# Kernel tuning notes

Measured on AMD Instinct MI355X. Metric: run time of the kernel, lower is better.

## Reference

```python
import jax, jax.numpy as jnp
import numpy as np

B, L, D = 2, 2048, 1024
H = 16
C = 128            # chunk_size
N = L // C         # num chunks
SCALE = float(np.sqrt(D))  # softmax_scale = sqrt(d_model)


def setup_inputs() -> dict:
    key = jax.random.key(0)
    ks = jax.random.split(key, 5)
    return {
        "x": jax.random.normal(ks[0], (B, L, D), dtype=jnp.float32),
        "w_qkv": jax.random.normal(ks[1], (D, 3 * D), dtype=jnp.float32) * (1.0 / np.sqrt(D)),
        "b_qkv": jax.random.normal(ks[2], (3 * D,), dtype=jnp.float32) * 0.02,
        "w_o": jax.random.normal(ks[3], (D, D), dtype=jnp.float32) * (1.0 / np.sqrt(D)),
        "b_o": jax.random.normal(ks[4], (D,), dtype=jnp.float32) * 0.02,
    }


def reference(x, w_qkv, b_qkv, w_o, b_o):
    b, l, d = x.shape
    hd = d // H
    qkv = x @ w_qkv + b_qkv                         # (B,L,3D)
    q, k, v = jnp.split(qkv, 3, axis=-1)
    q = q.reshape(b, l, H, hd)
    k = k.reshape(b, l, H, hd)
    v = v.reshape(b, l, H, hd)

    q_chunks = q.reshape(b, N, C, H, hd)
    k_chunks = k.reshape(b, N, C, H, hd)
    # mean_pool over the chunk dim
    q_pool = q_chunks.mean(axis=2)                  # (B,N,H,hd)
    k_pool = k_chunks.mean(axis=2)

    token2chunk = jnp.einsum('blhd,bnhd->bhln', q, k_pool)          # (B,H,L,N)
    chunk2token = jnp.einsum('bnhd,bnchd->bhnc', q_pool, k_chunks)  # (B,H,N,C)
    # outer product over (n,c) -> full (B,H,L,L) score matrix
    A = token2chunk[..., :, None] * chunk2token[:, :, None, :, :]   # (B,H,L,N,C)
    A = A.reshape(b, H, l, l)

    # direct intra-chunk attention overwrites the diagonal blocks
    direct = jnp.einsum('bnqhd,bnkhd->bhnqk', q_chunks, k_chunks)   # (B,H,N,C,C)
    A6 = A.reshape(b, H, N, C, N, C)
    eye = jnp.eye(N, dtype=bool)[:, None, :, None]                  # (N,1,N,1)
    A6 = jnp.where(eye, direct[:, :, :, :, None, :], A6)
    A = A6.reshape(b, H, l, l)

    # causal mask applied multiplicatively (masked scores become 0, NOT -inf)
    causal = jnp.tril(jnp.ones((l, l), dtype=bool))
    A = jnp.where(causal, A, 0.0) / SCALE
    A = jax.nn.softmax(A, axis=-1)

    out = jnp.einsum('bhqv,bvhd->bhqd', A, v)       # (B,H,L,hd)
    out = out.transpose(0, 2, 1, 3).reshape(b, l, d)
    return out @ w_o + b_o
```

## Files before the change

kernel.cpp:

```cpp
#include <hip/hip_runtime.h>
#include <math.h>

#define B_   2
#define L_   2048
#define D_   1024
#define H_   16
#define HD_  64
#define C_   128
#define N_   16
#define INV_SCALE 0.03125f

typedef _Float16 h8 __attribute__((ext_vector_type(8)));
typedef _Float16 h4 __attribute__((ext_vector_type(4)));
typedef float    f4 __attribute__((ext_vector_type(4)));

#define MFMA16(a, b, c) __builtin_amdgcn_mfma_f32_16x16x32_f16((a), (b), (c), 0, 0, 0)

__device__ __forceinline__ void gl_lds16(const void* g, void* l) {
  __builtin_amdgcn_global_load_lds(
      (const __attribute__((address_space(1))) void*)g,
      (__attribute__((address_space(3))) void*)l, 16, 0, 0);
}

__global__ __launch_bounds__(256) void cvtx_kernel(const float* __restrict__ X,
                                                   _Float16* __restrict__ Xh)
{
  int i = (blockIdx.x * 256 + threadIdx.x) * 4;
  float4 v = *(const float4*)(X + i);
  h4 o = { (_Float16)v.x, (_Float16)v.y, (_Float16)v.z, (_Float16)v.w };
  *(h4*)(Xh + i) = o;
}

__global__ __launch_bounds__(256) void wt_kernel(const float* __restrict__ W,
                                                 _Float16* __restrict__ WT,
                                                 int Nc, int Kd)
{
  __shared__ float ts[32][36];
  const int tid = threadIdx.x;
  const int n0 = blockIdx.x * 32, k0 = blockIdx.y * 32;
  {
    int kr = tid >> 3, nc4 = (tid & 7) * 4;
    float4 v = *(const float4*)&W[(size_t)(k0 + kr) * Nc + n0 + nc4];
    ts[kr][nc4+0] = v.x; ts[kr][nc4+1] = v.y; ts[kr][nc4+2] = v.z; ts[kr][nc4+3] = v.w;
  }
  __syncthreads();
  {
    int nr = tid >> 3, kc4 = (tid & 7) * 4;
    h4 o = { (_Float16)ts[kc4+0][nr], (_Float16)ts[kc4+1][nr],
             (_Float16)ts[kc4+2][nr], (_Float16)ts[kc4+3][nr] };
    *(h4*)&WT[(size_t)(n0 + nr) * Kd + k0 + kc4] = o;
  }
}

template<int MT>
__global__ __launch_bounds__(256, 4) void gemm16_kernel(
    const _Float16* __restrict__ A, const _Float16* __restrict__ Bt,
    const float* __restrict__ bias,
    _Float16* __restrict__ Qh, _Float16* __restrict__ Kh, _Float16* __restrict__ VT,
    float* __restrict__ out,
    float* __restrict__ QP, float* __restrict__ KP, float* __restrict__ VCS,
    int Kd, int mode)
{
  constexpr int SM = MT / 32;
  __shared__ __align__(16) _Float16 As[2][MT * 32];
  __shared__ __align__(16) _Float16 Bs[2][4096];
  __shared__ float cred[2][128];
  const int tid = threadIdx.x;
  const int lane = tid & 63, w = tid >> 6;
  const int q = lane >> 4, r = lane & 15;
  const int mb = (w >> 1) * (MT / 2);
  const int nb = (w & 1) * 64;

  int m0, n0;
  {
    const int id = blockIdx.x;
    const int xcd = id & 7, slot = id >> 3;
    if constexpr (MT == 128) {
      n0 = (xcd * 3 + (slot % 3)) * 128;
      m0 = (slot / 3) * 128;
    } else {
      n0 = xcd * 128;
      m0 = slot * 64;
    }
  }

  const int Rr = tid >> 2;
  const int cd = (tid & 3) ^ ((Rr >> 1) & 3);
  const _Float16* Ag = A + (size_t)(m0 + Rr) * Kd + cd * 8;
  const _Float16* Bg = Bt + (size_t)(n0 + Rr) * Kd + cd * 8;
  const size_t rowStep = (size_t)64 * Kd;

  f4 acc[SM][4];
  #pragma unroll
  for (int s = 0; s < SM; ++s)
    #pragma unroll
    for (int t = 0; t < 4; ++t) acc[s][t] = (f4){0.f, 0.f, 0.f, 0.f};

  const int nIter = Kd >> 5;
  const int koff = (q ^ ((r >> 1) & 3)) << 3;

  auto stage = [&](int bf, int kt) {
    _Float16* Asl = &As[bf][w * 512];
    _Float16* Bsl = &Bs[bf][w * 512];
    gl_lds16(Ag + kt, Asl);
    if constexpr (MT == 128) gl_lds16(Ag + kt + rowStep, Asl + 2048);
    gl_lds16(Bg + kt, Bsl);
    gl_lds16(Bg + kt + rowStep, Bsl + 2048);
  };

  stage(0, 0);

  for (int it = 0; it < nIter; ++it) {
    __syncthreads();
    if (it + 1 < nIter) stage((it + 1) & 1, (it + 1) << 5);
    const _Float16* Ab = As[it & 1];
    const _Float16* Bb = Bs[it & 1];
    h8 af[SM], bf4[4];
    #pragma unroll
    for (int s = 0; s < SM; ++s)
      af[s] = *(const h8*)&Ab[(mb + s * 16 + r) * 32 + koff];
    #pragma unroll
    for (int t = 0; t < 4; ++t)
      bf4[t] = *(const h8*)&Bb[(nb + t * 16 + r) * 32 + koff];
    #pragma unroll
    for (int s = 0; s < SM; ++s)
      #pragma unroll
      for (int t = 0; t < 4; ++t)
        acc[s][t] = MFMA16(af[s], bf4[t], acc[s][t]);
  }

  if (mode == 0) {
    #pragma unroll
    for (int t = 0; t < 4; ++t) {
      int gn = n0 + nb + t * 16 + r;
      float bj = bias[gn];
      int which = gn >> 10, rem = gn & 1023;
      int h2 = rem >> 6, d2 = rem & 63;
      if (which < 2) {
        _Float16* dst = which == 0 ? Qh : Kh;
        #pragma unroll
        for (int s = 0; s < SM; ++s)
          #pragma unroll
          for (int i = 0; i < 4; ++i) {
            int gm = m0 + mb + s * 16 + q * 4 + i;
            int b2 = gm >> 11, l2 = gm & 2047;
            dst[(((size_t)(b2 * H_ + h2)) * L_ + l2) * HD_ + d2] =
                (_Float16)(acc[s][t][i] + bj);
          }
      } else {
        #pragma unroll
        for (int s = 0; s < SM; ++s) {
          int gm0 = m0 + mb + s * 16 + q * 4;
          int b2 = gm0 >> 11, l2 = gm0 & 2047;
          h4 hv = { (_Float16)(acc[s][t][0] + bj), (_Float16)(acc[s][t][1] + bj),
                    (_Float16)(acc[s][t][2] + bj), (_Float16)(acc[s][t][3] + bj) };
          *(h4*)&VT[((size_t)(b2 * H_ + h2) * HD_ + d2) * L_ + l2] = hv;
        }
      }
    }
    float colsum[4];
    #pragma unroll
    for (int t = 0; t < 4; ++t) {
      float s2 = 0.f;
      #pragma unroll
      for (int s = 0; s < SM; ++s)
        #pragma unroll
        for (int i = 0; i < 4; ++i) s2 += acc[s][t][i];
      s2 += __shfl_xor(s2, 16);
      s2 += __shfl_xor(s2, 32);
      colsum[t] = s2;
    }
    if (q == 0) {
      #pragma unroll
      for (int t = 0; t < 4; ++t)
        cred[w >> 1][nb + t * 16 + r] = colsum[t];
    }
    __syncthreads();
    if (tid < 128) {
      int j = tid;
      float ssum = cred[0][j] + cred[1][j];
      int gn = n0 + j;
      float bj = bias[gn];
      int which = gn >> 10, rem = gn & 1023;
      int h2 = rem >> 6, d2 = rem & 63;
      int b2 = m0 >> 11, nch = (m0 & 2047) >> 7;
      size_t o = (((size_t)(b2 * H_ + h2)) * N_ + nch) * HD_ + d2;
      if (which == 0)      QP[o] = ssum * (1.f / 128.f) + bj;
      else if (which == 1) KP[o] = ssum * (1.f / 128.f) + bj;
      else                 VCS[o] = ssum + 128.f * bj;
    }
  } else {
    #pragma unroll
    for (int t = 0; t < 4; ++t) {
      int gn = n0 + nb + t * 16 + r;
      float bj = bias[gn];
      #pragma unroll
      for (int s = 0; s < SM; ++s)
        #pragma unroll
        for (int i = 0; i < 4; ++i) {
          int gm = m0 + mb + s * 16 + q * 4 + i;
          out[(size_t)gm * 1024 + gn] = acc[s][t][i] + bj;
        }
    }
  }
}

__global__ void csuf_kernel(const float* __restrict__ VCS, float* __restrict__ CSUF)
{
  int bh = blockIdx.x, d = threadIdx.x;
  float run = 0.f;
  for (int n = N_ - 1; n >= 0; --n) {
    size_t o = ((size_t)bh * N_ + n) * HD_ + d;
    CSUF[o] = run;
    run += VCS[o];
  }
}

__global__ __launch_bounds__(128) void c2t_kernel(
    const float* __restrict__ QP, const _Float16* __restrict__ Kh,
    float* __restrict__ C2T, float* __restrict__ C2TMX, float* __restrict__ C2TMN)
{
  __shared__ float qp_s[64];
  __shared__ float red[4];
  int bh = blockIdx.x >> 4, n = blockIdx.x & 15, tid = threadIdx.x;
  int w = tid >> 6, lane = tid & 63;
  if (tid < 64) qp_s[tid] = QP[((size_t)bh * N_ + n) * HD_ + tid];
  const _Float16* kr = Kh + (((size_t)bh * L_) + n * C_ + tid) * HD_;
  h8 kv[8];
  #pragma unroll
  for (int c8 = 0; c8 < 8; ++c8) kv[c8] = *(const h8*)(kr + c8 * 8);
  __syncthreads();
  float s = 0.f;
  #pragma unroll
  for (int c8 = 0; c8 < 8; ++c8)
    #pragma unroll
    for (int j = 0; j < 8; ++j)
      s = fmaf((float)kv[c8][j], qp_s[c8 * 8 + j], s);
  C2T[((size_t)bh * N_ + n) * C_ + tid] = s;
  float mx = s, mn = s;
  #pragma unroll
  for (int st = 1; st <= 32; st <<= 1) {
    mx = fmaxf(mx, __shfl_xor(mx, st));
    mn = fminf(mn, __shfl_xor(mn, st));
  }
  if (lane == 0) { red[w * 2] = mx; red[w * 2 + 1] = mn; }
  __syncthreads();
  if (tid == 0) {
    C2TMX[bh * N_ + n] = fmaxf(red[0], red[2]);
    C2TMN[bh * N_ + n] = fminf(red[1], red[3]);
  }
}

__global__ __launch_bounds__(256, 4) void attn3_kernel(
    const _Float16* __restrict__ Qh, const _Float16* __restrict__ Kh,
    const _Float16* __restrict__ VT,
    const float* __restrict__ C2T, const float* __restrict__ C2TMX,
    const float* __restrict__ C2TMN, const float* __restrict__ CSUF,
    const float* __restrict__ KP, _Float16* __restrict__ AOh)
{
  __shared__ __align__(16) _Float16 kv_s[2][8192];
  __shared__ __align__(16) _Float16 kp_s[1024];
  __shared__ __align__(16) float c2t_s[2][128];

  const int tid = threadIdx.x;
  const int w = tid >> 6, lane = tid & 63;
  const int q = lane >> 4, r = lane & 15;
  const int r7 = r & 7;
  const int id = blockIdx.x;
  const int bh = ((id & 7) << 2) + ((id >> 3) & 3);
  const int qt = 31 - (id >> 5);
  const int l0 = qt * 64;
  const int nq = l0 >> 7;
  const int off = l0 & 127;
  const int rowA = l0 + w * 16 + r;
  const int pcw = off + w * 16 + r;
  const size_t bhL = (size_t)bh * L_;
  const int b2 = bh >> 4, h2 = bh & 15;

  auto stageV = [&](int bf, int n) {
    #pragma unroll
    for (int j = 0; j < 4; ++j) {
      int f = j * 256 + tid;
      int d = f >> 4, p = f & 15;
      int c16 = p ^ (d & 7);
      gl_lds16(VT + ((size_t)bh * HD_ + d) * L_ + n * C_ + c16 * 8,
               &kv_s[bf][(size_t)(j * 256 + w * 64) * 8]);
    }
  };
  auto stageK = [&](int bf, int n) {
    #pragma unroll
    for (int j = 0; j < 4; ++j) {
      int f = j * 256 + tid;
      int c = f >> 3, p = f & 7;
      int ck = p ^ (c & 7);
      gl_lds16(Kh + (bhL + n * C_ + c) * HD_ + ck * 8,
               &kv_s[bf][(size_t)(j * 256 + w * 64) * 8]);
    }
  };
  auto stageC = [&](int bf, int n) {
    if (tid < 32)
      gl_lds16(C2T + ((size_t)bh * N_ + n) * C_ + lane * 4, &c2t_s[bf][0]);
  };

  {
    int n4 = tid >> 4, d4 = (tid & 15) * 4;
    float4 kpv = *(const float4*)&KP[((size_t)bh * N_ + n4) * HD_ + d4];
    int sd = ((((d4 >> 3) ^ (n4 & 7)) << 3) | (d4 & 7));
    h4 hv = { (_Float16)kpv.x, (_Float16)kpv.y, (_Float16)kpv.z, (_Float16)kpv.w };
    *(h4*)&kp_s[n4 * 64 + sd] = hv;
  }
  h8 qa0 = *(const h8*)(Qh + (bhL + rowA) * HD_ + q * 8);
  h8 qa1 = *(const h8*)(Qh + (bhL + rowA) * HD_ + 32 + q * 8);
  float mxL = C2TMX[bh * N_ + (lane & 15)];
  float mnL = C2TMN[bh * N_ + (lane & 15)];
  stageK(0, nq);
  __syncthreads();

  f4 tvacc = (f4){0.f, 0.f, 0.f, 0.f};
  {
    h8 kpa0 = *(const h8*)&kp_s[r * 64 + ((q ^ r7) << 3)];
    h8 kpa1 = *(const h8*)&kp_s[r * 64 + (((4 + q) ^ r7) << 3)];
    tvacc = MFMA16(kpa0, qa0, tvacc);
    tvacc = MFMA16(kpa1, qa1, tvacc);
  }
  float tvs[4];
  #pragma unroll
  for (int i = 0; i < 4; ++i) tvs[i] = tvacc[i] * INV_SCALE;

  float pm = -1e30f;
  #pragma unroll
  for (int i = 0; i < 4; ++i) {
    int n = q * 4 + i;
    float mx = __shfl(mxL, n);
    float mn = __shfl(mnL, n);
    float cm = fmaxf(tvs[i] * mx, tvs[i] * mn);
    pm = (n < nq) ? fmaxf(pm, cm) : pm;
  }
  pm = fmaxf(pm, __shfl_xor(pm, 16));
  pm = fmaxf(pm, __shfl_xor(pm, 32));

  f4 sc[8];
  #pragma unroll
  for (int u = 0; u < 8; ++u) sc[u] = (f4){0.f, 0.f, 0.f, 0.f};
  #pragma unroll
  for (int u = 0; u < 8; ++u) {
    h8 kb0 = *(const h8*)&kv_s[0][(u * 16 + r) * 64 + ((q ^ r7) << 3)];
    h8 kb1 = *(const h8*)&kv_s[0][(u * 16 + r) * 64 + (((4 + q) ^ r7) << 3)];
    sc[u] = MFMA16(qa0, kb0, sc[u]);
    sc[u] = MFMA16(qa1, kb1, sc[u]);
  }
  stageV(1, nq);

  float rm[4] = {-1e30f, -1e30f, -1e30f, -1e30f};
  #pragma unroll
  for (int u = 0; u < 8; ++u) {
    int col = nq * C_ + u * 16 + r;
    #pragma unroll
    for (int i = 0; i < 4; ++i) {
      int row = l0 + w * 16 + q * 4 + i;
      float v = sc[u][i] * INV_SCALE;
      v = (col <= row) ? v : -1e30f;
      sc[u][i] = v;
      rm[i] = fmaxf(rm[i], v);
    }
  }
  #pragma unroll
  for (int i = 0; i < 4; ++i) {
    rm[i] = fmaxf(rm[i], __shfl_xor(rm[i], 1));
    rm[i] = fmaxf(rm[i], __shfl_xor(rm[i], 2));
    rm[i] = fmaxf(rm[i], __shfl_xor(rm[i], 4));
    rm[i] = fmaxf(rm[i], __shfl_xor(rm[i], 8));
  }
  const int srcl = (r >> 2) << 4;
  const int ri = r & 3;
  float t0 = __shfl(rm[0], srcl), t1 = __shfl(rm[1], srcl);
  float t2 = __shfl(rm[2], srcl), t3 = __shfl(rm[3], srcl);
  float myrm = ri == 0 ? t0 : ri == 1 ? t1 : ri == 2 ? t2 : t3;

  const float M = fmaxf(fmaxf(pm, myrm), 0.f);
  const float e0 = __expf(-M);
  float Mc[4];
  #pragma unroll
  for (int i = 0; i < 4; ++i) Mc[i] = __shfl(M, (q << 2) + i);

  float cs[4] = {0.f, 0.f, 0.f, 0.f};
  #pragma unroll
  for (int u = 0; u < 8; ++u)
    #pragma unroll
    for (int i = 0; i < 4; ++i) {
      float v = sc[u][i];
      float p = (v > -1e29f) ? __expf(v - Mc[i]) : 0.f;
      sc[u][i] = p;
      cs[i] += p;
    }
  #pragma unroll
  for (int i = 0; i < 4; ++i) {
    cs[i] += __shfl_xor(cs[i], 1);
    cs[i] += __shfl_xor(cs[i], 2);
    cs[i] += __shfl_xor(cs[i], 4);
    cs[i] += __shfl_xor(cs[i], 8);
  }
  float c0 = __shfl(cs[0], srcl), c1 = __shfl(cs[1], srcl);
  float c2 = __shfl(cs[2], srcl), c3 = __shfl(cs[3], srcl);
  float den = ri == 0 ? c0 : ri == 1 ? c1 : ri == 2 ? c2 : c3;

  __syncthreads();
  _Float16* pw = &kv_s[0][w * 2048];
  #pragma unroll
  for (int u = 0; u < 8; ++u)
    #pragma unroll
    for (int i = 0; i < 4; ++i) {
      int row = q * 4 + i, col = u * 16 + r;
      pw[row * 128 + ((((col >> 3) ^ (row & 7)) << 3) | (col & 7))] =
          (_Float16)sc[u][i];
    }

  f4 oacc[4], sacc[4];
  #pragma unroll
  for (int t = 0; t < 4; ++t) {
    oacc[t] = (f4){0.f, 0.f, 0.f, 0.f};
    sacc[t] = (f4){0.f, 0.f, 0.f, 0.f};
  }
  #pragma unroll
  for (int s = 0; s < 4; ++s) {
    h8 pa = *(const h8*)&pw[r * 128 + (((s * 4 + q) ^ r7) << 3)];
    h8 mk;
    #pragma unroll
    for (int j2 = 0; j2 < 8; ++j2)
      mk[j2] = (_Float16)((s * 32 + q * 8 + j2 > pcw) ? 1.f : 0.f);
    #pragma unroll
    for (int t = 0; t < 4; ++t) {
      h8 vb = *(const h8*)&kv_s[1][(t * 16 + r) * 128 + (((s * 4 + q) ^ r7) << 3)];
      oacc[t] = MFMA16(pa, vb, oacc[t]);
      sacc[t] = MFMA16(mk, vb, sacc[t]);
    }
  }

  __syncthreads();
  if (nq >= 1) { stageV(0, nq - 1); stageC(0, nq - 1); }

  for (int n = nq - 1; n >= 0; --n) {
    const int cur = (nq - 1 - n) & 1, nxt = cur ^ 1;
    __syncthreads();
    if (n >= 1) { stageV(nxt, n - 1); stageC(nxt, n - 1); }
    int i0 = n & 3;
    float tvx = i0 == 0 ? tvs[0] : i0 == 1 ? tvs[1] : i0 == 2 ? tvs[2] : tvs[3];
    float tvn = __shfl(tvx, ((n >> 2) << 4) + r);
    float csum = 0.f;
    #pragma unroll
    for (int s = 0; s < 4; ++s) {
      const float* cp = &c2t_s[cur][s * 32 + q * 8];
      float4 ca = *(const float4*)cp;
      float4 cb = *(const float4*)(cp + 4);
      float p0 = __expf(tvn * ca.x - M), p1 = __expf(tvn * ca.y - M);
      float p2 = __expf(tvn * ca.z - M), p3 = __expf(tvn * ca.w - M);
      float p4 = __expf(tvn * cb.x - M), p5 = __expf(tvn * cb.y - M);
      float p6 = __expf(tvn * cb.z - M), p7 = __expf(tvn * cb.w - M);
      csum += p0 + p1 + p2 + p3 + p4 + p5 + p6 + p7;
      h8 pa = { (_Float16)p0, (_Float16)p1, (_Float16)p2, (_Float16)p3,
                (_Float16)p4, (_Float16)p5, (_Float16)p6, (_Float16)p7 };
      #pragma unroll
      for (int t = 0; t < 4; ++t) {
        h8 vb = *(const h8*)&kv_s[cur][(t * 16 + r) * 128 + (((s * 4 + q) ^ r7) << 3)];
        oacc[t] = MFMA16(pa, vb, oacc[t]);
      }
    }
    csum += __shfl_xor(csum, 16);
    csum += __shfl_xor(csum, 32);
    den += csum;
  }

  int cnt = (L_ - 1) - rowA;
  den += e0 * (float)cnt;
  float e0r[4], dnr[4];
  #pragma unroll
  for (int i = 0; i < 4; ++i) {
    e0r[i] = __shfl(e0,  (q << 2) + i);
    dnr[i] = __shfl(den, (q << 2) + i);
  }
  #pragma unroll
  for (int t = 0; t < 4; ++t) {
    int d = t * 16 + r;
    float csf = CSUF[((size_t)bh * N_ + nq) * HD_ + d];
    #pragma unroll
    for (int i = 0; i < 4; ++i) {
      int row = l0 + w * 16 + q * 4 + i;
      float suffix = sacc[t][i] + csf;
      float o = (oacc[t][i] + e0r[i] * suffix) / dnr[i];
      AOh[((size_t)b2 * L_ + row) * D_ + h2 * HD_ + d] = (_Float16)o;
    }
  }
}

extern "C" void kernel_launch(void* const* d_in, const int* in_sizes, int n_in,
                              void* d_out, int out_size, void* d_ws, size_t ws_size,
                              hipStream_t stream)
{
  (void)in_sizes; (void)n_in; (void)out_size; (void)ws_size;
  const float* x     = (const float*)d_in[0];
  const float* w_qkv = (const float*)d_in[1];
  const float* b_qkv = (const float*)d_in[2];
  const float* w_o   = (const float*)d_in[3];
  const float* b_o   = (const float*)d_in[4];
  float* out = (float*)d_out;

  char* p = (char*)d_ws;
  _Float16* xh   = (_Float16*)p; p += (size_t)4194304 * 2;
  _Float16* wqT  = (_Float16*)p; p += (size_t)3145728 * 2;
  _Float16* woT  = (_Float16*)p; p += (size_t)1048576 * 2;
  _Float16* Qh   = (_Float16*)p; p += (size_t)4194304 * 2;
  _Float16* Kh   = (_Float16*)p; p += (size_t)4194304 * 2;
  _Float16* VT   = (_Float16*)p; p += (size_t)4194304 * 2;
  _Float16* AOh  = (_Float16*)p; p += (size_t)4194304 * 2;
  float*    C2T  = (float*)p;    p += (size_t)65536 * 4;
  float*    QP   = (float*)p;    p += (size_t)32768 * 4;
  float*    KP   = (float*)p;    p += (size_t)32768 * 4;
  float*    VCS  = (float*)p;    p += (size_t)32768 * 4;
  float*    CSUF = (float*)p;    p += (size_t)32768 * 4;
  float*    MXa  = (float*)p;    p += (size_t)512 * 4;
  float*    MNa  = (float*)p;    p += (size_t)512 * 4;

  cvtx_kernel<<<4096, 256, 0, stream>>>(x, xh);
  wt_kernel<<<dim3(96, 32), 256, 0, stream>>>(w_qkv, wqT, 3 * D_, D_);
  wt_kernel<<<dim3(32, 32), 256, 0, stream>>>(w_o, woT, D_, D_);
  gemm16_kernel<128><<<768, 256, 0, stream>>>(
      xh, wqT, b_qkv, Qh, Kh, VT, nullptr, QP, KP, VCS, D_, 0);
  csuf_kernel<<<B_ * H_, 64, 0, stream>>>(VCS, CSUF);
  c2t_kernel<<<B_ * H_ * N_, 128, 0, stream>>>(QP, Kh, C2T, MXa, MNa);
  attn3_kernel<<<1024, 256, 0, stream>>>(
      Qh, Kh, VT, C2T, MXa, MNa, CSUF, KP, AOh);
  gemm16_kernel<64><<<512, 256, 0, stream>>>(
      AOh, woT, b_o, nullptr, nullptr, nullptr, out, nullptr, nullptr, nullptr, D_, 1);
}
```

Before: 180.8 us.

## Merge prep and pooling launches, widen attention blocks to full 128-row chunks

```diff
diff --git a/kernel.cpp b/kernel.cpp
--- a/kernel.cpp
+++ b/kernel.cpp
@@ -22,22 +22,30 @@
       (__attribute__((address_space(3))) void*)l, 16, 0, 0);
 }
 
-__global__ __launch_bounds__(256) void cvtx_kernel(const float* __restrict__ X,
-                                                   _Float16* __restrict__ Xh)
-{
-  int i = (blockIdx.x * 256 + threadIdx.x) * 4;
-  float4 v = *(const float4*)(X + i);
-  h4 o = { (_Float16)v.x, (_Float16)v.y, (_Float16)v.z, (_Float16)v.w };
-  *(h4*)(Xh + i) = o;
-}
-
-__global__ __launch_bounds__(256) void wt_kernel(const float* __restrict__ W,
-                                                 _Float16* __restrict__ WT,
-                                                 int Nc, int Kd)
+__global__ __launch_bounds__(256) void prep_kernel(
+    const float* __restrict__ X, _Float16* __restrict__ Xh,
+    const float* __restrict__ Wq, _Float16* __restrict__ WqT,
+    const float* __restrict__ Wo, _Float16* __restrict__ WoT)
 {
   __shared__ float ts[32][36];
   const int tid = threadIdx.x;
-  const int n0 = blockIdx.x * 32, k0 = blockIdx.y * 32;
+  const int id = blockIdx.x;
+  if (id < 4096) {
+    int i = id * 1024 + tid * 4;
+    float4 v = *(const float4*)(X + i);
+    h4 o = { (_Float16)v.x, (_Float16)v.y, (_Float16)v.z, (_Float16)v.w };
+    *(h4*)(Xh + i) = o;
+    return;
+  }
+  const float* W; _Float16* WT; int Nc, bx, by;
+  if (id < 7168) {
+    int idx = id - 4096;
+    W = Wq; WT = WqT; Nc = 3072; bx = idx % 96; by = idx / 96;
+  } else {
+    int idx = id - 7168;
+    W = Wo; WT = WoT; Nc = 1024; bx = idx & 31; by = idx >> 5;
+  }
+  const int n0 = bx * 32, k0 = by * 32;
   {
     int kr = tid >> 3, nc4 = (tid & 7) * 4;
     float4 v = *(const float4*)&W[(size_t)(k0 + kr) * Nc + n0 + nc4];
@@ -48,7 +56,7 @@
     int nr = tid >> 3, kc4 = (tid & 7) * 4;
     h4 o = { (_Float16)ts[kc4+0][nr], (_Float16)ts[kc4+1][nr],
              (_Float16)ts[kc4+2][nr], (_Float16)ts[kc4+3][nr] };
-    *(h4*)&WT[(size_t)(n0 + nr) * Kd + k0 + kc4] = o;
+    *(h4*)&WT[(size_t)(n0 + nr) * 1024 + k0 + kc4] = o;
   }
 }
 
@@ -177,9 +185,9 @@
     }
     __syncthreads();
     if (tid < 128) {
-      int j = tid;
-      float ssum = cred[0][j] + cred[1][j];
-      int gn = n0 + j;
+      int jj = tid;
+      float ssum = cred[0][jj] + cred[1][jj];
+      int gn = n0 + jj;
       float bj = bias[gn];
       int which = gn >> 10, rem = gn & 1023;
       int h2 = rem >> 6, d2 = rem & 63;
@@ -205,23 +213,26 @@
   }
 }
 
-__global__ void csuf_kernel(const float* __restrict__ VCS, float* __restrict__ CSUF)
-{
-  int bh = blockIdx.x, d = threadIdx.x;
-  float run = 0.f;
-  for (int n = N_ - 1; n >= 0; --n) {
-    size_t o = ((size_t)bh * N_ + n) * HD_ + d;
-    CSUF[o] = run;
-    run += VCS[o];
-  }
-}
-
-__global__ __launch_bounds__(128) void c2t_kernel(
+__global__ __launch_bounds__(128) void pool2_kernel(
     const float* __restrict__ QP, const _Float16* __restrict__ Kh,
-    float* __restrict__ C2T, float* __restrict__ C2TMX, float* __restrict__ C2TMN)
+    const float* __restrict__ VCS,
+    float* __restrict__ C2T, float* __restrict__ C2TMX, float* __restrict__ C2TMN,
+    float* __restrict__ CSUF)
 {
   __shared__ float qp_s[64];
   __shared__ float red[4];
+  if (blockIdx.x >= 512) {
+    int bh = blockIdx.x - 512, d = threadIdx.x;
+    if (d < 64) {
+      float run = 0.f;
+      for (int n = N_ - 1; n >= 0; --n) {
+        size_t o = ((size_t)bh * N_ + n) * HD_ + d;
+        CSUF[o] = run;
+        run += VCS[o];
+      }
+    }
+    return;
+  }
   int bh = blockIdx.x >> 4, n = blockIdx.x & 15, tid = threadIdx.x;
   int w = tid >> 6, lane = tid & 63;
   if (tid < 64) qp_s[tid] = QP[((size_t)bh * N_ + n) * HD_ + tid];
@@ -251,14 +262,16 @@
   }
 }
 
-__global__ __launch_bounds__(256, 4) void attn3_kernel(
+__global__ __launch_bounds__(512, 4) void attn4_kernel(
     const _Float16* __restrict__ Qh, const _Float16* __restrict__ Kh,
     const _Float16* __restrict__ VT,
     const float* __restrict__ C2T, const float* __restrict__ C2TMX,
     const float* __restrict__ C2TMN, const float* __restrict__ CSUF,
     const float* __restrict__ KP, _Float16* __restrict__ AOh)
 {
-  __shared__ __align__(16) _Float16 kv_s[2][8192];
+  __shared__ __align__(16) _Float16 buf0[8192];
+  __shared__ __align__(16) _Float16 buf1[8192];
+  __shared__ __align__(16) _Float16 buf2[8192];
   __shared__ __align__(16) _Float16 kp_s[1024];
   __shared__ __align__(16) float c2t_s[2][128];
 
@@ -268,41 +281,39 @@
   const int r7 = r & 7;
   const int id = blockIdx.x;
   const int bh = ((id & 7) << 2) + ((id >> 3) & 3);
-  const int qt = 31 - (id >> 5);
-  const int l0 = qt * 64;
-  const int nq = l0 >> 7;
-  const int off = l0 & 127;
+  const int nq = 15 - (id >> 5);
+  const int l0 = nq * 128;
   const int rowA = l0 + w * 16 + r;
-  const int pcw = off + w * 16 + r;
+  const int pcw = w * 16 + r;
   const size_t bhL = (size_t)bh * L_;
   const int b2 = bh >> 4, h2 = bh & 15;
 
-  auto stageV = [&](int bf, int n) {
-    #pragma unroll
-    for (int j = 0; j < 4; ++j) {
-      int f = j * 256 + tid;
+  auto stageV = [&](_Float16* buf, int n) {
+    #pragma unroll
+    for (int j2 = 0; j2 < 2; ++j2) {
+      int f = j2 * 512 + tid;
       int d = f >> 4, p = f & 15;
       int c16 = p ^ (d & 7);
       gl_lds16(VT + ((size_t)bh * HD_ + d) * L_ + n * C_ + c16 * 8,
-               &kv_s[bf][(size_t)(j * 256 + w * 64) * 8]);
+               buf + (size_t)(j2 * 512 + w * 64) * 8);
     }
   };
-  auto stageK = [&](int bf, int n) {
-    #pragma unroll
-    for (int j = 0; j < 4; ++j) {
-      int f = j * 256 + tid;
+  auto stageK = [&](_Float16* buf, int n) {
+    #pragma unroll
+    for (int j2 = 0; j2 < 2; ++j2) {
+      int f = j2 * 512 + tid;
       int c = f >> 3, p = f & 7;
       int ck = p ^ (c & 7);
       gl_lds16(Kh + (bhL + n * C_ + c) * HD_ + ck * 8,
-               &kv_s[bf][(size_t)(j * 256 + w * 64) * 8]);
+               buf + (size_t)(j2 * 512 + w * 64) * 8);
     }
   };
   auto stageC = [&](int bf, int n) {
     if (tid < 32)
-      gl_lds16(C2T + ((size_t)bh * N_ + n) * C_ + lane * 4, &c2t_s[bf][0]);
+      gl_lds16(C2T + ((size_t)bh * N_ + n) * C_ + tid * 4, &c2t_s[bf][0]);
   };
 
-  {
+  if (tid < 256) {
     int n4 = tid >> 4, d4 = (tid & 15) * 4;
     float4 kpv = *(const float4*)&KP[((size_t)bh * N_ + n4) * HD_ + d4];
     int sd = ((((d4 >> 3) ^ (n4 & 7)) << 3) | (d4 & 7));
@@ -311,9 +322,11 @@
   }
   h8 qa0 = *(const h8*)(Qh + (bhL + rowA) * HD_ + q * 8);
   h8 qa1 = *(const h8*)(Qh + (bhL + rowA) * HD_ + 32 + q * 8);
-  float mxL = C2TMX[bh * N_ + (lane & 15)];
-  float mnL = C2TMN[bh * N_ + (lane & 15)];
-  stageK(0, nq);
+  float mxL = C2TMX[bh * N_ + r];
+  float mnL = C2TMN[bh * N_ + r];
+  stageK(buf0, nq);
+  stageV(buf2, nq);
+  if (nq >= 1) stageC(0, nq - 1);
   __syncthreads();
 
   f4 tvacc = (f4){0.f, 0.f, 0.f, 0.f};
@@ -344,22 +357,21 @@
   for (int u = 0; u < 8; ++u) sc[u] = (f4){0.f, 0.f, 0.f, 0.f};
   #pragma unroll
   for (int u = 0; u < 8; ++u) {
-    h8 kb0 = *(const h8*)&kv_s[0][(u * 16 + r) * 64 + ((q ^ r7) << 3)];
-    h8 kb1 = *(const h8*)&kv_s[0][(u * 16 + r) * 64 + (((4 + q) ^ r7) << 3)];
+    h8 kb0 = *(const h8*)&buf0[(u * 16 + r) * 64 + ((q ^ r7) << 3)];
+    h8 kb1 = *(const h8*)&buf0[(u * 16 + r) * 64 + (((4 + q) ^ r7) << 3)];
     sc[u] = MFMA16(qa0, kb0, sc[u]);
     sc[u] = MFMA16(qa1, kb1, sc[u]);
   }
-  stageV(1, nq);
 
   float rm[4] = {-1e30f, -1e30f, -1e30f, -1e30f};
   #pragma unroll
   for (int u = 0; u < 8; ++u) {
-    int col = nq * C_ + u * 16 + r;
+    int lcol = u * 16 + r;
     #pragma unroll
     for (int i = 0; i < 4; ++i) {
-      int row = l0 + w * 16 + q * 4 + i;
+      int lrow = w * 16 + q * 4 + i;
       float v = sc[u][i] * INV_SCALE;
-      v = (col <= row) ? v : -1e30f;
+      v = (lcol <= lrow) ? v : -1e30f;
       sc[u][i] = v;
       rm[i] = fmaxf(rm[i], v);
     }
@@ -405,7 +417,8 @@
   float den = ri == 0 ? c0 : ri == 1 ? c1 : ri == 2 ? c2 : c3;
 
   __syncthreads();
-  _Float16* pw = &kv_s[0][w * 2048];
+
+  _Float16* pw = (w < 4) ? (buf0 + w * 2048) : (buf1 + (w - 4) * 2048);
   #pragma unroll
   for (int u = 0; u < 8; ++u)
     #pragma unroll
@@ -430,26 +443,31 @@
       mk[j2] = (_Float16)((s * 32 + q * 8 + j2 > pcw) ? 1.f : 0.f);
     #pragma unroll
     for (int t = 0; t < 4; ++t) {
-      h8 vb = *(const h8*)&kv_s[1][(t * 16 + r) * 128 + (((s * 4 + q) ^ r7) << 3)];
+      h8 vb = *(const h8*)&buf2[(t * 16 + r) * 128 + (((s * 4 + q) ^ r7) << 3)];
       oacc[t] = MFMA16(pa, vb, oacc[t]);
       sacc[t] = MFMA16(mk, vb, sacc[t]);
     }
   }
 
   __syncthreads();
-  if (nq >= 1) { stageV(0, nq - 1); stageC(0, nq - 1); }
+  if (nq >= 1) stageV(buf1, nq - 1);
 
   for (int n = nq - 1; n >= 0; --n) {
-    const int cur = (nq - 1 - n) & 1, nxt = cur ^ 1;
+    const int k = nq - 1 - n;
+    _Float16* curb = (k & 1) ? buf2 : buf1;
     __syncthreads();
-    if (n >= 1) { stageV(nxt, n - 1); stageC(nxt, n - 1); }
+    if (n >= 1) {
+      stageV((k & 1) ? buf1 : buf2, n - 1);
+      stageC((k + 1) & 1, n - 1);
+    }
     int i0 = n & 3;
     float tvx = i0 == 0 ? tvs[0] : i0 == 1 ? tvs[1] : i0 == 2 ? tvs[2] : tvs[3];
     float tvn = __shfl(tvx, ((n >> 2) << 4) + r);
     float csum = 0.f;
+    const float* c2p = c2t_s[k & 1];
     #pragma unroll
     for (int s = 0; s < 4; ++s) {
-      const float* cp = &c2t_s[cur][s * 32 + q * 8];
+      const float* cp = &c2p[s * 32 + q * 8];
       float4 ca = *(const float4*)cp;
       float4 cb = *(const float4*)(cp + 4);
       float p0 = __expf(tvn * ca.x - M), p1 = __expf(tvn * ca.y - M);
@@ -461,7 +479,7 @@
                 (_Float16)p4, (_Float16)p5, (_Float16)p6, (_Float16)p7 };
       #pragma unroll
       for (int t = 0; t < 4; ++t) {
-        h8 vb = *(const h8*)&kv_s[cur][(t * 16 + r) * 128 + (((s * 4 + q) ^ r7) << 3)];
+        h8 vb = *(const h8*)&curb[(t * 16 + r) * 128 + (((s * 4 + q) ^ r7) << 3)];
         oacc[t] = MFMA16(pa, vb, oacc[t]);
       }
     }
@@ -520,14 +538,11 @@
   float*    MXa  = (float*)p;    p += (size_t)512 * 4;
   float*    MNa  = (float*)p;    p += (size_t)512 * 4;
 
-  cvtx_kernel<<<4096, 256, 0, stream>>>(x, xh);
-  wt_kernel<<<dim3(96, 32), 256, 0, stream>>>(w_qkv, wqT, 3 * D_, D_);
-  wt_kernel<<<dim3(32, 32), 256, 0, stream>>>(w_o, woT, D_, D_);
+  prep_kernel<<<8192, 256, 0, stream>>>(x, xh, w_qkv, wqT, w_o, woT);
   gemm16_kernel<128><<<768, 256, 0, stream>>>(
       xh, wqT, b_qkv, Qh, Kh, VT, nullptr, QP, KP, VCS, D_, 0);
-  csuf_kernel<<<B_ * H_, 64, 0, stream>>>(VCS, CSUF);
-  c2t_kernel<<<B_ * H_ * N_, 128, 0, stream>>>(QP, Kh, C2T, MXa, MNa);
-  attn3_kernel<<<1024, 256, 0, stream>>>(
+  pool2_kernel<<<544, 128, 0, stream>>>(QP, Kh, VCS, C2T, MXa, MNa, CSUF);
+  attn4_kernel<<<512, 512, 0, stream>>>(
       Qh, Kh, VT, C2T, MXa, MNa, CSUF, KP, AOh);
   gemm16_kernel<64><<<512, 256, 0, stream>>>(
       AOh, woT, b_o, nullptr, nullptr, nullptr, out, nullptr, nullptr, nullptr, D_, 1);
```

Measured after the change: 179.8 us. Within noise of the previous version (-0.6%).
